# Kernel tuning notes

Hardware: AMD Instinct MI355X
Metric: run time of the kernel (lower is better)

The kernel has to match this reference:

```python
import jax, jax.numpy as jnp
import numpy as np

N_NODES = 50000
N_EDGES = 800000
IN_DIM = 96
HID_DIM = 96


def setup_inputs() -> dict:
    key = jax.random.key(0)
    ks = jax.random.split(key, 8)
    inputs = jax.random.normal(ks[0], (N_NODES, IN_DIM), dtype=jnp.float32)
    factor = jax.random.uniform(ks[1], (N_EDGES, 1), dtype=jnp.float32)
    src = jax.random.randint(ks[2], (N_EDGES,), 0, N_NODES, dtype=jnp.int32)
    dst = jax.random.randint(ks[3], (N_EDGES,), 0, N_NODES, dtype=jnp.int32)
    # Linear params (torch nn.Linear: y = x @ W.T + b), uniform(-1/sqrt(fan_in), ..)
    s1 = 1.0 / np.sqrt(IN_DIM)
    s2 = 1.0 / np.sqrt(HID_DIM)
    W1 = jax.random.uniform(ks[4], (HID_DIM, IN_DIM), minval=-s1, maxval=s1, dtype=jnp.float32)
    b1 = jax.random.uniform(ks[5], (HID_DIM,), minval=-s1, maxval=s1, dtype=jnp.float32)
    W2 = jax.random.uniform(ks[6], (IN_DIM, HID_DIM), minval=-s2, maxval=s2, dtype=jnp.float32)
    b2 = jax.random.uniform(ks[7], (IN_DIM,), minval=-s2, maxval=s2, dtype=jnp.float32)
    return {"inputs": inputs, "W1": W1, "b1": b1, "W2": W2, "b2": b2,
            "factor": factor, "src": src, "dst": dst}


def _propagate(feat, factor, src, dst, n_nodes):
    # message = h[src] * edge_factor ; reduce = sum at dst
    msg = feat[src] * factor                       # [E, D]
    return jax.ops.segment_sum(msg, dst, num_segments=n_nodes)


def reference(inputs, W1, b1, W2, b2, factor, src, dst):
    n = inputs.shape[0]
    # in-degree norm: deg^{-1/2}, clamped at 1
    deg = jax.ops.segment_sum(jnp.ones((src.shape[0],), inputs.dtype), dst,
                              num_segments=n)
    norm = jnp.maximum(deg, 1.0) ** -0.5           # [N]
    norm = norm[:, None]                           # [N, 1]

    feat = (inputs @ W1.T + b1) * norm             # [N, H]
    h = jnp.tanh(_propagate(feat, factor, src, dst, n))

    feat = (h @ W2.T + b2) * norm                  # [N, D]
    h = jnp.tanh(_propagate(feat, factor, src, dst, n))

    # dgl.mean_nodes over a single graph -> [1, D]; unsqueeze(-1) -> [1, D, 1]
    pooled = jnp.mean(h, axis=0, keepdims=True)[..., None]
    return jnp.tanh(pooled)
```

## Files before the change

kernel.cpp:

```cpp
#include <hip/hip_runtime.h>
#include <math.h>
#include <type_traits>

#define N_NODES 50000
#define N_EDGES 800000
#define DIM 96
#define BCH 12
#define SCAN_BLK 256
#define NBLK ((N_NODES + SCAN_BLK - 1) / SCAN_BLK)
#define NPB 21
#define NBG ((N_NODES + NPB - 1) / NPB)
#define CAP 768
#define R1_ROWS 24
#define R1_BLOCKS ((NBG + R1_ROWS - 1) / R1_ROWS)
#define SC_PASSES 4
#define SC_WIN ((N_NODES + SC_PASSES - 1) / SC_PASSES)
#define F8_SCALE 16.0f
#define F8_INV   0.0625f

typedef short v8s __attribute__((ext_vector_type(8)));
typedef float v4f __attribute__((ext_vector_type(4)));
typedef float v2f __attribute__((ext_vector_type(2)));

__device__ __forceinline__ unsigned short f2bf(float f) {
    unsigned int u = __float_as_uint(f);
    u += 0x7FFFu + ((u >> 16) & 1u);
    return (unsigned short)(u >> 16);
}
__device__ __forceinline__ unsigned int pack2bf(float lo, float hi) {
    return (unsigned int)f2bf(lo) | ((unsigned int)f2bf(hi) << 16);
}

__device__ __forceinline__ float fast_tanh(float x) {
    float ax = fabsf(x);
    float t = __expf(-2.0f * ax);
    float r = (1.0f - t) / (1.0f + t);
    return copysignf(r, x);
}

__device__ __forceinline__ void accf8(float* a, uint2 v, float f) {
    v2f p0 = __builtin_amdgcn_cvt_pk_f32_fp8(v.x, false);
    v2f p1 = __builtin_amdgcn_cvt_pk_f32_fp8(v.x, true);
    v2f p2 = __builtin_amdgcn_cvt_pk_f32_fp8(v.y, false);
    v2f p3 = __builtin_amdgcn_cvt_pk_f32_fp8(v.y, true);
    a[0] += p0.x * f; a[1] += p0.y * f;
    a[2] += p1.x * f; a[3] += p1.y * f;
    a[4] += p2.x * f; a[5] += p2.y * f;
    a[6] += p3.x * f; a[7] += p3.y * f;
}

union U4S8 { uint4 u; v8s s; };


__global__ void count_deg(const int* __restrict__ dst, int* __restrict__ deg,
                          int* __restrict__ rank) {
    int e = blockIdx.x * blockDim.x + threadIdx.x;
    if (e < N_EDGES) rank[e] = atomicAdd(&deg[dst[e]], 1);
}

__global__ void deg_partials(const int* __restrict__ deg, float* __restrict__ norm,
                             int* __restrict__ partials) {
    int b = blockIdx.x, t = threadIdx.x;
    int n = b * SCAN_BLK + t;
    int v = 0;
    if (n < N_NODES) {
        v = deg[n];
        norm[n] = rsqrtf(fmaxf((float)v, 1.0f));
    }
    int s = v;
#pragma unroll
    for (int off = 32; off > 0; off >>= 1) s += __shfl_down(s, off, 64);
    __shared__ int ws_[4];
    if ((t & 63) == 0) ws_[t >> 6] = s;
    __syncthreads();
    if (t == 0) partials[b] = ws_[0] + ws_[1] + ws_[2] + ws_[3];
}

__global__ void scan_partials(const int* __restrict__ partials, int* __restrict__ pprefix) {
    __shared__ int sm[SCAN_BLK];
    int t = threadIdx.x;
    int v = (t < NBLK) ? partials[t] : 0;
    sm[t] = v;
    __syncthreads();
    for (int off = 1; off < SCAN_BLK; off <<= 1) {
        int u = (t >= off) ? sm[t - off] : 0;
        __syncthreads();
        sm[t] += u;
        __syncthreads();
    }
    if (t < NBLK) pprefix[t] = sm[t] - v;
}

__global__ void make_offsets(const int* __restrict__ deg, const int* __restrict__ pprefix,
                             int* __restrict__ offs) {
    __shared__ int sm[SCAN_BLK];
    int b = blockIdx.x, t = threadIdx.x;
    int idx = b * SCAN_BLK + t;
    int v = (idx < N_NODES) ? deg[idx] : 0;
    sm[t] = v;
    __syncthreads();
    for (int off = 1; off < SCAN_BLK; off <<= 1) {
        int u = (t >= off) ? sm[t - off] : 0;
        __syncthreads();
        sm[t] += u;
        __syncthreads();
    }
    if (idx < N_NODES) offs[idx] = pprefix[b] + sm[t] - v;
    if (b == 0 && t == 0) offs[N_NODES] = N_EDGES;
}

__global__ void scatter_edges(const int* __restrict__ src, const int* __restrict__ dst,
                              const float* __restrict__ factor, const int* __restrict__ rank,
                              const int* __restrict__ offs, int2* __restrict__ entries) {
    int tid0 = blockIdx.x * blockDim.x + threadIdx.x;
    int stride = gridDim.x * blockDim.x;
#pragma unroll 1
    for (int pass = 0; pass < SC_PASSES; ++pass) {
        int lo = pass * SC_WIN;
        int hi = min(lo + SC_WIN, N_NODES);
#pragma unroll 1
        for (int e = tid0; e < N_EDGES; e += stride) {
            int d = dst[e];
            if (d >= lo && d < hi) {
                int pos = offs[d] + rank[e];
                entries[pos] = make_int2(src[e], __float_as_int(factor[e]));
            }
        }
    }
}


__global__ void swizzle_W(const float* __restrict__ W, uint4* __restrict__ bsw) {
    int idx = blockIdx.x * blockDim.x + threadIdx.x;
    if (idx >= 18 * 64) return;
    int t = idx >> 6, lane = idx & 63;
    int kt = t / 6, jt = t % 6;
    int quad = lane >> 4, l16 = lane & 15;
    const float4* wp = (const float4*)(W + (size_t)(jt * 16 + l16) * DIM + kt * 32 + quad * 8);
    float4 w0 = wp[0], w1 = wp[1];
    bsw[idx] = make_uint4(pack2bf(w0.x, w0.y), pack2bf(w0.z, w0.w),
                          pack2bf(w1.x, w1.y), pack2bf(w1.z, w1.w));
}


template <typename T>
__global__ __launch_bounds__(256) void gemm_mfma(const T* __restrict__ X,
                                                 const uint4* __restrict__ bsw,
                                                 const float* __restrict__ bias,
                                                 const float* __restrict__ norm,
                                                 unsigned char* __restrict__ out) {
    int tid = threadIdx.x;
    int wave = tid >> 6, lane = tid & 63;
    int quad = lane >> 4, l16 = lane & 15;
    int n0 = blockIdx.x * 64 + wave * 16;
    int node = n0 + l16;
    int rowc = min(node, N_NODES - 1);

    uint4 bfr[18];
#pragma unroll
    for (int t = 0; t < 18; ++t) bfr[t] = bsw[t * 64 + lane];

    v4f acc[6];
#pragma unroll
    for (int jt = 0; jt < 6; ++jt) acc[jt] = (v4f)(0.0f);

#pragma unroll
    for (int kt = 0; kt < 3; ++kt) {
        U4S8 x;
        if constexpr (std::is_same_v<T, float>) {
            const float4* xp = (const float4*)(X + (size_t)rowc * DIM + kt * 32 + quad * 8);
            float4 x0 = xp[0], x1 = xp[1];
            x.u = make_uint4(pack2bf(x0.x, x0.y), pack2bf(x0.z, x0.w),
                             pack2bf(x1.x, x1.y), pack2bf(x1.z, x1.w));
        } else {
            x.u = *(const uint4*)(X + (size_t)rowc * DIM + kt * 32 + quad * 8);
        }
#pragma unroll
        for (int jt = 0; jt < 6; ++jt) {
            U4S8 w; w.u = bfr[kt * 6 + jt];
            acc[jt] = __builtin_amdgcn_mfma_f32_16x16x32_bf16(w.s, x.s, acc[jt], 0, 0, 0);
        }
    }

    if (node < N_NODES) {
        float nm = norm[node] * F8_SCALE;
#pragma unroll
        for (int jt = 0; jt < 6; ++jt) {
            float4 bj = *(const float4*)(bias + jt * 16 + quad * 4);
            float v0 = (acc[jt][0] + bj.x) * nm;
            float v1 = (acc[jt][1] + bj.y) * nm;
            float v2 = (acc[jt][2] + bj.z) * nm;
            float v3 = (acc[jt][3] + bj.w) * nm;
            unsigned int w = (unsigned int)__builtin_amdgcn_cvt_pk_fp8_f32(v0, v1, 0, false);
            w = (unsigned int)__builtin_amdgcn_cvt_pk_fp8_f32(v2, v3, (int)w, true);
            *(unsigned int*)(out + (size_t)node * DIM + jt * 16 + quad * 4) = w;
        }
    }
}


template <bool POOL>
__global__ void gather_agg_f8(const unsigned char* __restrict__ feat,
                              const int* __restrict__ offs,
                              const int2* __restrict__ entries,
                              unsigned short* __restrict__ out,
                              float* __restrict__ partials) {
    __shared__ int2 ents[CAP];
    __shared__ float pool[DIM];
    __shared__ int sh_base, sh_cnt;
    int tid = threadIdx.x;
    int n0 = blockIdx.x * NPB;
    int n1 = min(n0 + NPB, N_NODES);
    if (POOL && tid < DIM) pool[tid] = 0.f;
    if (tid == 0) { sh_base = offs[n0]; sh_cnt = offs[n1] - sh_base; }
    __syncthreads();
    int base = sh_base, cnt = sh_cnt;

    int nl = tid / BCH;
    int c  = tid - nl * BCH;
    int n  = n0 + nl;
    bool active = (tid < NPB * BCH) && (n < N_NODES);
    int lb = 0, le = 0;
    if (active) { lb = offs[n] - base; le = offs[n + 1] - base; }

    float a0[8], a1[8];
#pragma unroll
    for (int i = 0; i < 8; ++i) { a0[i] = 0.f; a1[i] = 0.f; }

    for (int tb = 0; tb < cnt; tb += CAP) {
        int tcnt = min(cnt - tb, CAP);
        if (tb) __syncthreads();
        for (int i = tid; i < tcnt; i += 256) ents[i] = entries[base + tb + i];
        __syncthreads();
        int s = max(lb - tb, 0), e = min(le - tb, tcnt);
        int p = s;
        for (; p + 7 < e; p += 8) {
            int2 q0 = ents[p + 0], q1 = ents[p + 1], q2 = ents[p + 2], q3 = ents[p + 3];
            int2 q4 = ents[p + 4], q5 = ents[p + 5], q6 = ents[p + 6], q7 = ents[p + 7];
            uint2 v0 = *((const uint2*)(feat + (size_t)q0.x * DIM) + c);
            uint2 v1 = *((const uint2*)(feat + (size_t)q1.x * DIM) + c);
            uint2 v2 = *((const uint2*)(feat + (size_t)q2.x * DIM) + c);
            uint2 v3 = *((const uint2*)(feat + (size_t)q3.x * DIM) + c);
            uint2 v4 = *((const uint2*)(feat + (size_t)q4.x * DIM) + c);
            uint2 v5 = *((const uint2*)(feat + (size_t)q5.x * DIM) + c);
            uint2 v6 = *((const uint2*)(feat + (size_t)q6.x * DIM) + c);
            uint2 v7 = *((const uint2*)(feat + (size_t)q7.x * DIM) + c);
            accf8(a0, v0, __int_as_float(q0.y));
            accf8(a1, v1, __int_as_float(q1.y));
            accf8(a0, v2, __int_as_float(q2.y));
            accf8(a1, v3, __int_as_float(q3.y));
            accf8(a0, v4, __int_as_float(q4.y));
            accf8(a1, v5, __int_as_float(q5.y));
            accf8(a0, v6, __int_as_float(q6.y));
            accf8(a1, v7, __int_as_float(q7.y));
        }
        for (; p + 3 < e; p += 4) {
            int2 q0 = ents[p], q1 = ents[p + 1], q2 = ents[p + 2], q3 = ents[p + 3];
            uint2 v0 = *((const uint2*)(feat + (size_t)q0.x * DIM) + c);
            uint2 v1 = *((const uint2*)(feat + (size_t)q1.x * DIM) + c);
            uint2 v2 = *((const uint2*)(feat + (size_t)q2.x * DIM) + c);
            uint2 v3 = *((const uint2*)(feat + (size_t)q3.x * DIM) + c);
            accf8(a0, v0, __int_as_float(q0.y));
            accf8(a1, v1, __int_as_float(q1.y));
            accf8(a0, v2, __int_as_float(q2.y));
            accf8(a1, v3, __int_as_float(q3.y));
        }
        for (; p < e; ++p) {
            int2 q0 = ents[p];
            uint2 v0 = *((const uint2*)(feat + (size_t)q0.x * DIM) + c);
            accf8(a0, v0, __int_as_float(q0.y));
        }
    }

#pragma unroll
    for (int i = 0; i < 8; ++i) a0[i] = fast_tanh((a0[i] + a1[i]) * F8_INV);
    if (!POOL) {
        if (active) {
            uint4 o;
            o.x = pack2bf(a0[0], a0[1]);
            o.y = pack2bf(a0[2], a0[3]);
            o.z = pack2bf(a0[4], a0[5]);
            o.w = pack2bf(a0[6], a0[7]);
            ((uint4*)out)[n * BCH + c] = o;
        }
    } else {
        if (active) {
#pragma unroll
            for (int i = 0; i < 8; ++i) atomicAdd(&pool[c * 8 + i], a0[i]);
        }
        __syncthreads();
        if (tid < DIM) partials[(size_t)blockIdx.x * DIM + tid] = pool[tid];
    }
}


__global__ void reduce_stage1(const float* __restrict__ poolpart, float* __restrict__ stage1) {
    __shared__ float pool[DIM];
    int b = blockIdx.x, t = threadIdx.x;
    if (t < DIM) pool[t] = 0.f;
    __syncthreads();
    const int base = b * R1_ROWS * DIM;
    float loc = 0.f;
    int lastc = -1;
    for (int i = t; i < R1_ROWS * DIM; i += 256) {
        int gi = base + i;
        if (gi < NBG * DIM) {
            int col = i % DIM;
            if (col != lastc) {
                if (lastc >= 0) atomicAdd(&pool[lastc], loc);
                lastc = col; loc = 0.f;
            }
            loc += poolpart[gi];
        }
    }
    if (lastc >= 0) atomicAdd(&pool[lastc], loc);
    __syncthreads();
    if (t < DIM) stage1[b * DIM + t] = pool[t];
}

__global__ void reduce_stage2(const float* __restrict__ stage1, float* __restrict__ out) {
    __shared__ float sm[960];
    int t = threadIdx.x;
    int col = t % DIM, slice = t / DIM;
    float s = 0.f;
    for (int k = slice; k < R1_BLOCKS; k += 10) s += stage1[k * DIM + col];
    sm[t] = s;
    __syncthreads();
    if (t < DIM) {
        float tot = 0.f;
#pragma unroll
        for (int i = 0; i < 10; ++i) tot += sm[i * DIM + t];
        out[t] = tanhf(tot * (1.0f / N_NODES));
    }
}


extern "C" void kernel_launch(void* const* d_in, const int* in_sizes, int n_in,
                              void* d_out, int out_size, void* d_ws, size_t ws_size,
                              hipStream_t stream) {
    const float* inputs = (const float*)d_in[0];
    const float* W1     = (const float*)d_in[1];
    const float* b1     = (const float*)d_in[2];
    const float* W2     = (const float*)d_in[3];
    const float* b2     = (const float*)d_in[4];
    const float* factor = (const float*)d_in[5];
    const int*   src    = (const int*)d_in[6];
    const int*   dst    = (const int*)d_in[7];
    float* out = (float*)d_out;

    char* ws = (char*)d_ws;
    int*            deg      = (int*)(ws + 0);
    int*            rank     = (int*)(ws + 262144);
    int*            offs     = (int*)(ws + 3932160);
    float*          norm     = (float*)(ws + 4194304);
    int*            partials = (int*)(ws + 4456448);
    int*            pprefix  = (int*)(ws + 4458496);
    int2*           entries  = (int2*)(ws + 4718592);
    unsigned char*  bufA     = (unsigned char*)(ws + 11534336);
    unsigned short* bufB     = (unsigned short*)(ws + 21364736);
    float*          poolpart = (float*)(ws + 31195136);
    float*          stage1   = (float*)(ws + 32145536);
    uint4*          bsw1     = (uint4*)(ws + 33554432);
    uint4*          bsw2     = (uint4*)(ws + 33574912);

    swizzle_W<<<5, 256, 0, stream>>>(W1, bsw1);
    swizzle_W<<<5, 256, 0, stream>>>(W2, bsw2);

    hipMemsetAsync(deg, 0, N_NODES * sizeof(int), stream);
    count_deg<<<(N_EDGES + 255) / 256, 256, 0, stream>>>(dst, deg, rank);
    deg_partials<<<NBLK, SCAN_BLK, 0, stream>>>(deg, norm, partials);
    scan_partials<<<1, SCAN_BLK, 0, stream>>>(partials, pprefix);
    make_offsets<<<NBLK, SCAN_BLK, 0, stream>>>(deg, pprefix, offs);
    scatter_edges<<<2048, 256, 0, stream>>>(src, dst, factor, rank, offs, entries);

    const int GEMM_BLOCKS = (N_NODES + 63) / 64;

    gemm_mfma<float><<<GEMM_BLOCKS, 256, 0, stream>>>(inputs, bsw1, b1, norm, bufA);
    gather_agg_f8<false><<<NBG, 256, 0, stream>>>(bufA, offs, entries, bufB, nullptr);

    gemm_mfma<unsigned short><<<GEMM_BLOCKS, 256, 0, stream>>>(bufB, bsw2, b2, norm, bufA);
    gather_agg_f8<true><<<NBG, 256, 0, stream>>>(bufA, offs, entries, nullptr, poolpart);

    reduce_stage1<<<R1_BLOCKS, 256, 0, stream>>>(poolpart, stage1);
    reduce_stage2<<<1, 960, 0, stream>>>(stage1, out);
}
```

Measured before the change: 232.6 us.

## Fuse graph build into one persistent kernel with grid barriers; fuse pooling reduction

Merges weight swizzle, degree counting, the two-level scan, offset construction and edge scatter into a single 256-block persistent kernel that separates phases with software grid barriers (atomic counter plus spin-wait). The final pooling reduction is folded into the last gather kernel through global atomics and a last-block-done counter that applies the tanh. This removes about eight kernel launches and a memset, cutting launch gaps. In exchange, the count and scatter phases run on a smaller grid, and the grid barrier assumes all 256 blocks are resident at once.

```diff
diff --git a/kernel.cpp b/kernel.cpp
--- a/kernel.cpp
+++ b/kernel.cpp
@@ -6,17 +6,15 @@
 #define N_EDGES 800000
 #define DIM 96
 #define BCH 12
-#define SCAN_BLK 256
-#define NBLK ((N_NODES + SCAN_BLK - 1) / SCAN_BLK)
 #define NPB 21
 #define NBG ((N_NODES + NPB - 1) / NPB)
 #define CAP 768
-#define R1_ROWS 24
-#define R1_BLOCKS ((NBG + R1_ROWS - 1) / R1_ROWS)
 #define SC_PASSES 4
 #define SC_WIN ((N_NODES + SC_PASSES - 1) / SC_PASSES)
 #define F8_SCALE 16.0f
 #define F8_INV   0.0625f
+#define NB 256
+#define CHUNK ((N_NODES + NB - 1) / NB)
 
 typedef short v8s __attribute__((ext_vector_type(8)));
 typedef float v4f __attribute__((ext_vector_type(4)));
@@ -52,74 +50,91 @@
 union U4S8 { uint4 u; v8s s; };
 
 
-__global__ void count_deg(const int* __restrict__ dst, int* __restrict__ deg,
-                          int* __restrict__ rank) {
-    int e = blockIdx.x * blockDim.x + threadIdx.x;
-    if (e < N_EDGES) rank[e] = atomicAdd(&deg[dst[e]], 1);
-}
-
-__global__ void deg_partials(const int* __restrict__ deg, float* __restrict__ norm,
-                             int* __restrict__ partials) {
+__device__ __forceinline__ void gbar(int* cnt, int k) {
+    __syncthreads();
+    if (threadIdx.x == 0) {
+        __threadfence();
+        atomicAdd(&cnt[k], 1);
+        while (__hip_atomic_load(&cnt[k], __ATOMIC_ACQUIRE, __HIP_MEMORY_SCOPE_AGENT) < NB) {
+            __builtin_amdgcn_s_sleep(8);
+        }
+    }
+    __syncthreads();
+}
+
+__global__ __launch_bounds__(256) void build_all(
+        const int* __restrict__ src, const int* __restrict__ dst,
+        const float* __restrict__ factor,
+        const float* __restrict__ W1, const float* __restrict__ W2,
+        uint4* __restrict__ bsw1, uint4* __restrict__ bsw2,
+        int* __restrict__ deg, int* __restrict__ rank, int* __restrict__ offs,
+        float* __restrict__ norm, int* __restrict__ partials,
+        int* __restrict__ bar, float* __restrict__ gpool, int* __restrict__ done_cnt,
+        int2* __restrict__ entries) {
     int b = blockIdx.x, t = threadIdx.x;
-    int n = b * SCAN_BLK + t;
+    int gtid = b * 256 + t;
+    const int GSZ = NB * 256;
+
+    for (int n = gtid; n < N_NODES; n += GSZ) deg[n] = 0;
+    if (gtid < DIM) gpool[gtid] = 0.f;
+    if (gtid == DIM) *done_cnt = 0;
+    if (gtid < 2 * 1152) {
+        int w = gtid / 1152, idx = gtid % 1152;
+        const float* W = w ? W2 : W1;
+        uint4* bsw = w ? bsw2 : bsw1;
+        int t18 = idx >> 6, lane = idx & 63;
+        int kt = t18 / 6, jt = t18 % 6;
+        int quad = lane >> 4, l16 = lane & 15;
+        const float4* wp = (const float4*)(W + (size_t)(jt * 16 + l16) * DIM + kt * 32 + quad * 8);
+        float4 w0 = wp[0], w1 = wp[1];
+        bsw[idx] = make_uint4(pack2bf(w0.x, w0.y), pack2bf(w0.z, w0.w),
+                              pack2bf(w1.x, w1.y), pack2bf(w1.z, w1.w));
+    }
+    gbar(bar, 0);
+
+    for (int e = gtid; e < N_EDGES; e += GSZ) rank[e] = atomicAdd(&deg[dst[e]], 1);
+    gbar(bar, 1);
+
+    __shared__ int sm[256];
+    int node = b * CHUNK + t;
     int v = 0;
-    if (n < N_NODES) {
-        v = deg[n];
-        norm[n] = rsqrtf(fmaxf((float)v, 1.0f));
-    }
-    int s = v;
-#pragma unroll
-    for (int off = 32; off > 0; off >>= 1) s += __shfl_down(s, off, 64);
-    __shared__ int ws_[4];
-    if ((t & 63) == 0) ws_[t >> 6] = s;
-    __syncthreads();
-    if (t == 0) partials[b] = ws_[0] + ws_[1] + ws_[2] + ws_[3];
-}
-
-__global__ void scan_partials(const int* __restrict__ partials, int* __restrict__ pprefix) {
-    __shared__ int sm[SCAN_BLK];
-    int t = threadIdx.x;
-    int v = (t < NBLK) ? partials[t] : 0;
+    if (t < CHUNK && node < N_NODES) {
+        v = deg[node];
+        norm[node] = rsqrtf(fmaxf((float)v, 1.0f));
+    }
     sm[t] = v;
     __syncthreads();
-    for (int off = 1; off < SCAN_BLK; off <<= 1) {
+    for (int off = 1; off < 256; off <<= 1) {
         int u = (t >= off) ? sm[t - off] : 0;
         __syncthreads();
         sm[t] += u;
         __syncthreads();
     }
-    if (t < NBLK) pprefix[t] = sm[t] - v;
-}
-
-__global__ void make_offsets(const int* __restrict__ deg, const int* __restrict__ pprefix,
-                             int* __restrict__ offs) {
-    __shared__ int sm[SCAN_BLK];
-    int b = blockIdx.x, t = threadIdx.x;
-    int idx = b * SCAN_BLK + t;
-    int v = (idx < N_NODES) ? deg[idx] : 0;
-    sm[t] = v;
-    __syncthreads();
-    for (int off = 1; off < SCAN_BLK; off <<= 1) {
+    int my_excl = sm[t] - v;
+    if (t == 0) partials[b] = sm[255];
+    gbar(bar, 2);
+
+    int pv = partials[t];
+    __syncthreads();
+    sm[t] = pv;
+    __syncthreads();
+    for (int off = 1; off < 256; off <<= 1) {
         int u = (t >= off) ? sm[t - off] : 0;
         __syncthreads();
         sm[t] += u;
         __syncthreads();
     }
-    if (idx < N_NODES) offs[idx] = pprefix[b] + sm[t] - v;
+    int ppfx = (b > 0) ? sm[b - 1] : 0;
+    if (t < CHUNK && node < N_NODES) offs[node] = ppfx + my_excl;
     if (b == 0 && t == 0) offs[N_NODES] = N_EDGES;
-}
-
-__global__ void scatter_edges(const int* __restrict__ src, const int* __restrict__ dst,
-                              const float* __restrict__ factor, const int* __restrict__ rank,
-                              const int* __restrict__ offs, int2* __restrict__ entries) {
-    int tid0 = blockIdx.x * blockDim.x + threadIdx.x;
-    int stride = gridDim.x * blockDim.x;
+    gbar(bar, 3);
+
 #pragma unroll 1
     for (int pass = 0; pass < SC_PASSES; ++pass) {
         int lo = pass * SC_WIN;
         int hi = min(lo + SC_WIN, N_NODES);
 #pragma unroll 1
-        for (int e = tid0; e < N_EDGES; e += stride) {
+        for (int e = gtid; e < N_EDGES; e += GSZ) {
             int d = dst[e];
             if (d >= lo && d < hi) {
                 int pos = offs[d] + rank[e];
@@ -127,19 +142,6 @@
             }
         }
     }
-}
-
-
-__global__ void swizzle_W(const float* __restrict__ W, uint4* __restrict__ bsw) {
-    int idx = blockIdx.x * blockDim.x + threadIdx.x;
-    if (idx >= 18 * 64) return;
-    int t = idx >> 6, lane = idx & 63;
-    int kt = t / 6, jt = t % 6;
-    int quad = lane >> 4, l16 = lane & 15;
-    const float4* wp = (const float4*)(W + (size_t)(jt * 16 + l16) * DIM + kt * 32 + quad * 8);
-    float4 w0 = wp[0], w1 = wp[1];
-    bsw[idx] = make_uint4(pack2bf(w0.x, w0.y), pack2bf(w0.z, w0.w),
-                          pack2bf(w1.x, w1.y), pack2bf(w1.z, w1.w));
 }
 
 
@@ -204,10 +206,12 @@
                               const int* __restrict__ offs,
                               const int2* __restrict__ entries,
                               unsigned short* __restrict__ out,
-                              float* __restrict__ partials) {
+                              float* __restrict__ gpool,
+                              int* __restrict__ done_cnt,
+                              float* __restrict__ final_out) {
     __shared__ int2 ents[CAP];
     __shared__ float pool[DIM];
-    __shared__ int sh_base, sh_cnt;
+    __shared__ int sh_base, sh_cnt, sh_last;
     int tid = threadIdx.x;
     int n0 = blockIdx.x * NPB;
     int n1 = min(n0 + NPB, N_NODES);
@@ -289,48 +293,18 @@
             for (int i = 0; i < 8; ++i) atomicAdd(&pool[c * 8 + i], a0[i]);
         }
         __syncthreads();
-        if (tid < DIM) partials[(size_t)blockIdx.x * DIM + tid] = pool[tid];
-    }
-}
-
-
-__global__ void reduce_stage1(const float* __restrict__ poolpart, float* __restrict__ stage1) {
-    __shared__ float pool[DIM];
-    int b = blockIdx.x, t = threadIdx.x;
-    if (t < DIM) pool[t] = 0.f;
-    __syncthreads();
-    const int base = b * R1_ROWS * DIM;
-    float loc = 0.f;
-    int lastc = -1;
-    for (int i = t; i < R1_ROWS * DIM; i += 256) {
-        int gi = base + i;
-        if (gi < NBG * DIM) {
-            int col = i % DIM;
-            if (col != lastc) {
-                if (lastc >= 0) atomicAdd(&pool[lastc], loc);
-                lastc = col; loc = 0.f;
-            }
-            loc += poolpart[gi];
-        }
-    }
-    if (lastc >= 0) atomicAdd(&pool[lastc], loc);
-    __syncthreads();
-    if (t < DIM) stage1[b * DIM + t] = pool[t];
-}
-
-__global__ void reduce_stage2(const float* __restrict__ stage1, float* __restrict__ out) {
-    __shared__ float sm[960];
-    int t = threadIdx.x;
-    int col = t % DIM, slice = t / DIM;
-    float s = 0.f;
-    for (int k = slice; k < R1_BLOCKS; k += 10) s += stage1[k * DIM + col];
-    sm[t] = s;
-    __syncthreads();
-    if (t < DIM) {
-        float tot = 0.f;
-#pragma unroll
-        for (int i = 0; i < 10; ++i) tot += sm[i * DIM + t];
-        out[t] = tanhf(tot * (1.0f / N_NODES));
+        if (tid < DIM) atomicAdd(&gpool[tid], pool[tid]);
+        __threadfence();
+        if (tid == 0) {
+            int old = atomicAdd(done_cnt, 1);
+            sh_last = (old == NBG - 1);
+        }
+        __syncthreads();
+        if (sh_last && tid < DIM) {
+            float v = __hip_atomic_load(&gpool[tid], __ATOMIC_ACQUIRE,
+                                        __HIP_MEMORY_SCOPE_AGENT);
+            final_out[tid] = tanhf(v * (1.0f / N_NODES));
+        }
     }
 }
 
@@ -351,36 +325,31 @@
     char* ws = (char*)d_ws;
     int*            deg      = (int*)(ws + 0);
     int*            rank     = (int*)(ws + 262144);
-    int*            offs     = (int*)(ws + 3932160);
-    float*          norm     = (float*)(ws + 4194304);
-    int*            partials = (int*)(ws + 4456448);
-    int*            pprefix  = (int*)(ws + 4458496);
-    int2*           entries  = (int2*)(ws + 4718592);
+    int*            offs     = (int*)(ws + 3670016);
+    float*          norm     = (float*)(ws + 3932160);
+    int*            partials = (int*)(ws + 4194304);
+    int*            bar      = (int*)(ws + 4196352);
+    float*          gpool    = (float*)(ws + 4196416);
+    int*            done_cnt = (int*)(ws + 4196800);
+    int2*           entries  = (int2*)(ws + 4456448);
     unsigned char*  bufA     = (unsigned char*)(ws + 11534336);
-    unsigned short* bufB     = (unsigned short*)(ws + 21364736);
-    float*          poolpart = (float*)(ws + 31195136);
-    float*          stage1   = (float*)(ws + 32145536);
-    uint4*          bsw1     = (uint4*)(ws + 33554432);
-    uint4*          bsw2     = (uint4*)(ws + 33574912);
-
-    swizzle_W<<<5, 256, 0, stream>>>(W1, bsw1);
-    swizzle_W<<<5, 256, 0, stream>>>(W2, bsw2);
-
-    hipMemsetAsync(deg, 0, N_NODES * sizeof(int), stream);
-    count_deg<<<(N_EDGES + 255) / 256, 256, 0, stream>>>(dst, deg, rank);
-    deg_partials<<<NBLK, SCAN_BLK, 0, stream>>>(deg, norm, partials);
-    scan_partials<<<1, SCAN_BLK, 0, stream>>>(partials, pprefix);
-    make_offsets<<<NBLK, SCAN_BLK, 0, stream>>>(deg, pprefix, offs);
-    scatter_edges<<<2048, 256, 0, stream>>>(src, dst, factor, rank, offs, entries);
+    unsigned short* bufB     = (unsigned short*)(ws + 16777216);
+    uint4*          bsw1     = (uint4*)(ws + 26738688);
+    uint4*          bsw2     = (uint4*)(ws + 26759168);
+
+    hipMemsetAsync(bar, 0, 64, stream);
+
+    build_all<<<NB, 256, 0, stream>>>(src, dst, factor, W1, W2, bsw1, bsw2,
+                                      deg, rank, offs, norm, partials,
+                                      bar, gpool, done_cnt, entries);
 
     const int GEMM_BLOCKS = (N_NODES + 63) / 64;
 
     gemm_mfma<float><<<GEMM_BLOCKS, 256, 0, stream>>>(inputs, bsw1, b1, norm, bufA);
-    gather_agg_f8<false><<<NBG, 256, 0, stream>>>(bufA, offs, entries, bufB, nullptr);
+    gather_agg_f8<false><<<NBG, 256, 0, stream>>>(bufA, offs, entries, bufB,
+                                                  nullptr, nullptr, nullptr);
 
     gemm_mfma<unsigned short><<<GEMM_BLOCKS, 256, 0, stream>>>(bufB, bsw2, b2, norm, bufA);
-    gather_agg_f8<true><<<NBG, 256, 0, stream>>>(bufA, offs, entries, nullptr, poolpart);
-
-    reduce_stage1<<<R1_BLOCKS, 256, 0, stream>>>(poolpart, stage1);
-    reduce_stage2<<<1, 960, 0, stream>>>(stage1, out);
-}
+    gather_agg_f8<true><<<NBG, 256, 0, stream>>>(bufA, offs, entries, nullptr,
+                                                 gpool, done_cnt, out);
+}
```

Result: slower. 437.2 us (+87.9%).

## Fuse prep and scan kernels via grid barrier, merge final reductions

Applied to the files above, without the earlier changes.

Merges the two weight-swizzle kernels and the three-kernel degree scan into one kernel that uses a software grid barrier across its 196 blocks, and folds the two-stage final reduction into one kernel where the last-finishing block computes the output. A single memset now zeroes the degree array together with the barrier and done counters. This removes about five kernel launches and their inter-kernel gaps. The software barrier depends on all 196 blocks being resident at once, which holds on this GPU but is not guaranteed by the programming model.

```diff
diff --git a/kernel.cpp b/kernel.cpp
--- a/kernel.cpp
+++ b/kernel.cpp
@@ -58,28 +58,46 @@
     if (e < N_EDGES) rank[e] = atomicAdd(&deg[dst[e]], 1);
 }
 
-__global__ void deg_partials(const int* __restrict__ deg, float* __restrict__ norm,
-                             int* __restrict__ partials) {
+__device__ __forceinline__ void gbar(int* cnt, int k, int nb) {
+    __syncthreads();
+    if (threadIdx.x == 0) {
+        __threadfence();
+        atomicAdd(&cnt[k], 1);
+        while (__hip_atomic_load(&cnt[k], __ATOMIC_ACQUIRE, __HIP_MEMORY_SCOPE_AGENT) < nb) {
+            __builtin_amdgcn_s_sleep(8);
+        }
+    }
+    __syncthreads();
+}
+
+__global__ __launch_bounds__(256) void scan_all(
+        const float* __restrict__ W1, const float* __restrict__ W2,
+        uint4* __restrict__ bsw1, uint4* __restrict__ bsw2,
+        const int* __restrict__ deg, float* __restrict__ norm,
+        int* __restrict__ partials, int* __restrict__ bar, int* __restrict__ offs) {
     int b = blockIdx.x, t = threadIdx.x;
-    int n = b * SCAN_BLK + t;
+    int gtid = b * 256 + t;
+
+    if (gtid < 2 * 1152) {
+        int w = gtid / 1152, idx = gtid % 1152;
+        const float* W = w ? W2 : W1;
+        uint4* bsw = w ? bsw2 : bsw1;
+        int t18 = idx >> 6, lane = idx & 63;
+        int kt = t18 / 6, jt = t18 % 6;
+        int quad = lane >> 4, l16 = lane & 15;
+        const float4* wp = (const float4*)(W + (size_t)(jt * 16 + l16) * DIM + kt * 32 + quad * 8);
+        float4 w0 = wp[0], w1 = wp[1];
+        bsw[idx] = make_uint4(pack2bf(w0.x, w0.y), pack2bf(w0.z, w0.w),
+                              pack2bf(w1.x, w1.y), pack2bf(w1.z, w1.w));
+    }
+
+    __shared__ int sm[SCAN_BLK];
+    int idx = b * SCAN_BLK + t;
     int v = 0;
-    if (n < N_NODES) {
-        v = deg[n];
-        norm[n] = rsqrtf(fmaxf((float)v, 1.0f));
-    }
-    int s = v;
-#pragma unroll
-    for (int off = 32; off > 0; off >>= 1) s += __shfl_down(s, off, 64);
-    __shared__ int ws_[4];
-    if ((t & 63) == 0) ws_[t >> 6] = s;
-    __syncthreads();
-    if (t == 0) partials[b] = ws_[0] + ws_[1] + ws_[2] + ws_[3];
-}
-
-__global__ void scan_partials(const int* __restrict__ partials, int* __restrict__ pprefix) {
-    __shared__ int sm[SCAN_BLK];
-    int t = threadIdx.x;
-    int v = (t < NBLK) ? partials[t] : 0;
+    if (idx < N_NODES) {
+        v = deg[idx];
+        norm[idx] = rsqrtf(fmaxf((float)v, 1.0f));
+    }
     sm[t] = v;
     __syncthreads();
     for (int off = 1; off < SCAN_BLK; off <<= 1) {
@@ -88,16 +106,13 @@
         sm[t] += u;
         __syncthreads();
     }
-    if (t < NBLK) pprefix[t] = sm[t] - v;
-}
-
-__global__ void make_offsets(const int* __restrict__ deg, const int* __restrict__ pprefix,
-                             int* __restrict__ offs) {
-    __shared__ int sm[SCAN_BLK];
-    int b = blockIdx.x, t = threadIdx.x;
-    int idx = b * SCAN_BLK + t;
-    int v = (idx < N_NODES) ? deg[idx] : 0;
-    sm[t] = v;
+    int my_excl = sm[t] - v;
+    if (t == 0) partials[b] = sm[SCAN_BLK - 1];
+    gbar(bar, 0, NBLK);
+
+    int pv = (t < NBLK) ? partials[t] : 0;
+    __syncthreads();
+    sm[t] = pv;
     __syncthreads();
     for (int off = 1; off < SCAN_BLK; off <<= 1) {
         int u = (t >= off) ? sm[t - off] : 0;
@@ -105,7 +120,8 @@
         sm[t] += u;
         __syncthreads();
     }
-    if (idx < N_NODES) offs[idx] = pprefix[b] + sm[t] - v;
+    int ppfx = (b > 0) ? sm[b - 1] : 0;
+    if (idx < N_NODES) offs[idx] = ppfx + my_excl;
     if (b == 0 && t == 0) offs[N_NODES] = N_EDGES;
 }
 
@@ -127,19 +143,6 @@
             }
         }
     }
-}
-
-
-__global__ void swizzle_W(const float* __restrict__ W, uint4* __restrict__ bsw) {
-    int idx = blockIdx.x * blockDim.x + threadIdx.x;
-    if (idx >= 18 * 64) return;
-    int t = idx >> 6, lane = idx & 63;
-    int kt = t / 6, jt = t % 6;
-    int quad = lane >> 4, l16 = lane & 15;
-    const float4* wp = (const float4*)(W + (size_t)(jt * 16 + l16) * DIM + kt * 32 + quad * 8);
-    float4 w0 = wp[0], w1 = wp[1];
-    bsw[idx] = make_uint4(pack2bf(w0.x, w0.y), pack2bf(w0.z, w0.w),
-                          pack2bf(w1.x, w1.y), pack2bf(w1.z, w1.w));
 }
 
 
@@ -294,8 +297,10 @@
 }
 
 
-__global__ void reduce_stage1(const float* __restrict__ poolpart, float* __restrict__ stage1) {
+__global__ void reduce_all(const float* __restrict__ poolpart, float* __restrict__ stage1,
+                           int* __restrict__ done_cnt, float* __restrict__ out) {
     __shared__ float pool[DIM];
+    __shared__ int sh_last;
     int b = blockIdx.x, t = threadIdx.x;
     if (t < DIM) pool[t] = 0.f;
     __syncthreads();
@@ -316,21 +321,19 @@
     if (lastc >= 0) atomicAdd(&pool[lastc], loc);
     __syncthreads();
     if (t < DIM) stage1[b * DIM + t] = pool[t];
-}
-
-__global__ void reduce_stage2(const float* __restrict__ stage1, float* __restrict__ out) {
-    __shared__ float sm[960];
-    int t = threadIdx.x;
-    int col = t % DIM, slice = t / DIM;
-    float s = 0.f;
-    for (int k = slice; k < R1_BLOCKS; k += 10) s += stage1[k * DIM + col];
-    sm[t] = s;
-    __syncthreads();
-    if (t < DIM) {
-        float tot = 0.f;
-#pragma unroll
-        for (int i = 0; i < 10; ++i) tot += sm[i * DIM + t];
-        out[t] = tanhf(tot * (1.0f / N_NODES));
+    __threadfence();
+    __syncthreads();
+    if (t == 0) sh_last = (atomicAdd(done_cnt, 1) == R1_BLOCKS - 1);
+    __syncthreads();
+    if (sh_last) {
+        __threadfence();
+        if (t < DIM) {
+            float s = 0.f;
+            for (int k = 0; k < R1_BLOCKS; ++k)
+                s += __hip_atomic_load(&stage1[k * DIM + t], __ATOMIC_ACQUIRE,
+                                       __HIP_MEMORY_SCOPE_AGENT);
+            out[t] = tanhf(s * (1.0f / N_NODES));
+        }
     }
 }
 
@@ -350,27 +353,25 @@
 
     char* ws = (char*)d_ws;
     int*            deg      = (int*)(ws + 0);
+    int*            bar      = (int*)(ws + 204800);
+    int*            done_cnt = (int*)(ws + 204864);
     int*            rank     = (int*)(ws + 262144);
-    int*            offs     = (int*)(ws + 3932160);
-    float*          norm     = (float*)(ws + 4194304);
-    int*            partials = (int*)(ws + 4456448);
-    int*            pprefix  = (int*)(ws + 4458496);
-    int2*           entries  = (int2*)(ws + 4718592);
+    int*            offs     = (int*)(ws + 3670016);
+    float*          norm     = (float*)(ws + 3932160);
+    int*            partials = (int*)(ws + 4194304);
+    int2*           entries  = (int2*)(ws + 4456448);
     unsigned char*  bufA     = (unsigned char*)(ws + 11534336);
-    unsigned short* bufB     = (unsigned short*)(ws + 21364736);
-    float*          poolpart = (float*)(ws + 31195136);
-    float*          stage1   = (float*)(ws + 32145536);
-    uint4*          bsw1     = (uint4*)(ws + 33554432);
-    uint4*          bsw2     = (uint4*)(ws + 33574912);
-
-    swizzle_W<<<5, 256, 0, stream>>>(W1, bsw1);
-    swizzle_W<<<5, 256, 0, stream>>>(W2, bsw2);
-
-    hipMemsetAsync(deg, 0, N_NODES * sizeof(int), stream);
+    unsigned short* bufB     = (unsigned short*)(ws + 16777216);
+    float*          poolpart = (float*)(ws + 26738688);
+    float*          stage1   = (float*)(ws + 27787264);
+    uint4*          bsw1     = (uint4*)(ws + 27836416);
+    uint4*          bsw2     = (uint4*)(ws + 27856896);
+
+    hipMemsetAsync(ws, 0, 204928, stream);
+
     count_deg<<<(N_EDGES + 255) / 256, 256, 0, stream>>>(dst, deg, rank);
-    deg_partials<<<NBLK, SCAN_BLK, 0, stream>>>(deg, norm, partials);
-    scan_partials<<<1, SCAN_BLK, 0, stream>>>(partials, pprefix);
-    make_offsets<<<NBLK, SCAN_BLK, 0, stream>>>(deg, pprefix, offs);
+    scan_all<<<NBLK, SCAN_BLK, 0, stream>>>(W1, W2, bsw1, bsw2, deg, norm,
+                                            partials, bar, offs);
     scatter_edges<<<2048, 256, 0, stream>>>(src, dst, factor, rank, offs, entries);
 
     const int GEMM_BLOCKS = (N_NODES + 63) / 64;
@@ -381,6 +382,5 @@
     gemm_mfma<unsigned short><<<GEMM_BLOCKS, 256, 0, stream>>>(bufB, bsw2, b2, norm, bufA);
     gather_agg_f8<true><<<NBG, 256, 0, stream>>>(bufA, offs, entries, nullptr, poolpart);
 
-    reduce_stage1<<<R1_BLOCKS, 256, 0, stream>>>(poolpart, stage1);
-    reduce_stage2<<<1, 960, 0, stream>>>(stage1, out);
-}
+    reduce_all<<<R1_BLOCKS, 256, 0, stream>>>(poolpart, stage1, done_cnt, out);
+}
```

After: 263.5 us. +13.3%, slower.
